# Kernel tuning notes

Hardware: AMD Instinct MI355X
Metric: run time of the kernel (lower is better)

The kernel has to match this reference:

```python
import jax, jax.numpy as jnp
import numpy as np

C = 256
C8 = C // 8


def setup_inputs() -> dict:
    key = jax.random.key(0)
    ks = jax.random.split(key, 9)
    B, H, W = 4, 64, 64
    s = 1.0 / np.sqrt(C)
    return {
        "pre_feat": jax.random.normal(ks[0], (B, C, H, W), jnp.float32),
        "post_feat": jax.random.normal(ks[1], (B, C, H, W), jnp.float32),
        "Wq": jax.random.normal(ks[2], (C8, C), jnp.float32) * s,
        "bq": jnp.zeros((C8,), jnp.float32),
        "Wk": jax.random.normal(ks[3], (C8, C), jnp.float32) * s,
        "bk": jnp.zeros((C8,), jnp.float32),
        "Wv": jax.random.normal(ks[4], (C, C), jnp.float32) * s,
        "bv": jnp.zeros((C,), jnp.float32),
        "gamma": jnp.zeros((1,), jnp.float32),
    }


def reference(pre_feat, post_feat, Wq, bq, Wk, bk, Wv, bv, gamma):
    B, Cc, H, W = pre_feat.shape
    N = H * W
    pre = pre_feat.reshape(B, Cc, N)    # (B, C, N)
    post = post_feat.reshape(B, Cc, N)
    # 1x1 convs == per-pixel linear projections
    q = jnp.einsum('dc,bcn->bdn', Wq, post) + bq[None, :, None]  # (B, C8, N)
    k = jnp.einsum('dc,bcn->bdn', Wk, pre) + bk[None, :, None]   # (B, C8, N)
    v = jnp.einsum('dc,bcn->bdn', Wv, pre) + bv[None, :, None]   # (B, C, N)
    # energy[b,i,j] = <q[b,:,i], k[b,:,j]>  (unscaled)
    energy = jnp.einsum('bdi,bdj->bij', q, k)                    # (B, N, N)
    attention = jax.nn.softmax(energy, axis=-1)
    # out[b,c,i] = sum_j v[b,c,j] * attention[b,i,j]
    out = jnp.einsum('bcj,bij->bci', v, attention).reshape(B, Cc, H, W)
    return gamma[0] * out + post_feat
```

## Files before the change

kernel.cpp:

```cpp
#include <hip/hip_runtime.h>
#include <hip/hip_bf16.h>

#define Bn 4
#define Cn 256
#define Dn 32
#define Nn 4096

typedef __bf16 bf16x8 __attribute__((ext_vector_type(8)));
typedef float f32x4 __attribute__((ext_vector_type(4)));

__device__ __forceinline__ float bf2f(unsigned short u) {
  unsigned int v = ((unsigned int)u) << 16;
  return __builtin_bit_cast(float, v);
}
__device__ __forceinline__ unsigned short f2bf(float f) {
  unsigned int v = __builtin_bit_cast(unsigned int, f);
  v += 0x7FFFu + ((v >> 16) & 1u);
  return (unsigned short)(v >> 16);
}
__device__ __forceinline__ unsigned int pk2(float a, float b) {
  union { __hip_bfloat162 h; unsigned int u; } x;
  x.h = __float22bfloat162_rn(make_float2(a, b));
  return x.u;
}
__device__ __forceinline__ bf16x8 ldfrag(const unsigned short* p) {
  return __builtin_bit_cast(bf16x8, *(const uint4*)p);
}
__device__ __forceinline__ bf16x8 ldfrag_f32(const float* p) {
  float4 a = *(const float4*)p;
  float4 b = *(const float4*)(p + 4);
  union { unsigned int u2[4]; bf16x8 v; } x;
  x.u2[0] = pk2(a.x, a.y); x.u2[1] = pk2(a.z, a.w);
  x.u2[2] = pk2(b.x, b.y); x.u2[3] = pk2(b.z, b.w);
  return x.v;
}
__device__ __forceinline__ void async16(unsigned short* lds, const unsigned short* g) {
  __builtin_amdgcn_global_load_lds(
      (const __attribute__((address_space(1))) unsigned int*)g,
      (__attribute__((address_space(3))) unsigned int*)lds, 16, 0, 0);
}

__global__ __launch_bounds__(256) void qkprep(
    const float* __restrict__ pre, const float* __restrict__ post,
    const float* __restrict__ Wq, const float* __restrict__ bq,
    const float* __restrict__ Wk, const float* __restrict__ bk,
    const float* __restrict__ Wv, const float* __restrict__ bv,
    unsigned short* __restrict__ Qt, unsigned short* __restrict__ Kt,
    unsigned short* __restrict__ VBf)
{
  const int blk = blockIdx.x, tid = threadIdx.x;
  const int lane = tid & 63, w = tid >> 6;
  const int quad = lane >> 4, n16 = lane & 15;
  const f32x4 zz = {0.f, 0.f, 0.f, 0.f};

  if (blk >= 512) {
    __shared__ __align__(16) unsigned short sV[256 * 40];
    const int vb = blk - 512;
    const int b = vb >> 7;
    const int j0 = (vb & 127) << 5;
    const int jsub = w & 1, chalf = w >> 1;
    const int j = j0 + jsub * 16 + n16;

    f32x4 acc[8];
#pragma unroll
    for (int ct = 0; ct < 8; ct++) acc[ct] = zz;

    const float* preB = pre + (size_t)b * Cn * Nn + j;
#pragma unroll
    for (int kc = 0; kc < 8; kc++) {
      const float* pr = preB + (size_t)(kc * 32 + quad * 8) * Nn;
      union { unsigned int u2[4]; bf16x8 v; } bp;
#pragma unroll
      for (int e2 = 0; e2 < 4; e2++) {
        float r0 = pr[(size_t)(2 * e2) * Nn], r1 = pr[(size_t)(2 * e2 + 1) * Nn];
        bp.u2[e2] = pk2(r0, r1);
      }
#pragma unroll
      for (int ct = 0; ct < 8; ct++) {
        bf16x8 aw = ldfrag_f32(Wv + (size_t)(chalf * 128 + ct * 16 + n16) * Cn + kc * 32 + quad * 8);
        acc[ct] = __builtin_amdgcn_mfma_f32_16x16x32_bf16(aw, bp.v, acc[ct], 0, 0, 0);
      }
    }
#pragma unroll
    for (int ct = 0; ct < 8; ct++) {
#pragma unroll
      for (int r = 0; r < 4; r++) {
        const int c = chalf * 128 + ct * 16 + quad * 4 + r;
        sV[c * 40 + jsub * 16 + n16] = f2bf(acc[ct][r] + bv[c]);
      }
    }
    __syncthreads();
#pragma unroll
    for (int k = 0; k < 4; k++) {
      const int slot = tid + k * 256;
      const int c = slot >> 2, seg = slot & 3;
      *(uint4*)(VBf + ((size_t)b * Cn + c) * Nn + j0 + seg * 8) =
          *(const uint4*)(sV + c * 40 + seg * 8);
    }
    return;
  }

  const int b = blk >> 7;
  const int i0 = (blk & 127) << 5;
  const int isub = w & 1, dh = w >> 1;
  const int i = i0 + isub * 16 + n16;

  f32x4 aq = zz, ak = zz;
  const float* postB = post + (size_t)b * Cn * Nn + i;
  const float* preB  = pre  + (size_t)b * Cn * Nn + i;

#pragma unroll
  for (int kc = 0; kc < 8; kc++) {
    const int c0 = kc * 32 + quad * 8;
    const float* pp = postB + (size_t)c0 * Nn;
    const float* pr = preB + (size_t)c0 * Nn;
    union { unsigned int u2[4]; bf16x8 v; } bp, bq8;
#pragma unroll
    for (int e2 = 0; e2 < 4; e2++) {
      float p0 = pp[(size_t)(2 * e2) * Nn], p1 = pp[(size_t)(2 * e2 + 1) * Nn];
      float r0 = pr[(size_t)(2 * e2) * Nn], r1 = pr[(size_t)(2 * e2 + 1) * Nn];
      bp.u2[e2] = pk2(p0, p1);
      bq8.u2[e2] = pk2(r0, r1);
    }
    bf16x8 awq = ldfrag_f32(Wq + (size_t)(dh * 16 + n16) * Cn + kc * 32 + quad * 8);
    bf16x8 awk = ldfrag_f32(Wk + (size_t)(dh * 16 + n16) * Cn + kc * 32 + quad * 8);
    aq = __builtin_amdgcn_mfma_f32_16x16x32_bf16(awq, bp.v, aq, 0, 0, 0);
    ak = __builtin_amdgcn_mfma_f32_16x16x32_bf16(awk, bq8.v, ak, 0, 0, 0);
  }
  const float LOG2E = 1.44269504f;
  union { unsigned short s[4]; uint2 u; } oq, ok;
#pragma unroll
  for (int r = 0; r < 4; r++) {
    int d = dh * 16 + quad * 4 + r;
    oq.s[r] = f2bf((aq[r] + bq[d]) * LOG2E);
    ok.s[r] = f2bf(ak[r] + bk[d]);
  }
  *(uint2*)(Qt + ((size_t)b * Nn + i) * Dn + dh * 16 + quad * 4) = oq.u;
  *(uint2*)(Kt + ((size_t)b * Nn + i) * Dn + dh * 16 + quad * 4) = ok.u;
}

__global__ __launch_bounds__(256, 4) void flash_attn(
    const unsigned short* __restrict__ Qt, const unsigned short* __restrict__ Kt,
    const unsigned short* __restrict__ VBf,
    unsigned short* __restrict__ Opart, float* __restrict__ Lpart)
{
  __shared__ __align__(16) unsigned short sX[256 * 64];
  __shared__ __align__(16) unsigned short Pl[64 * 64];

  const int tid = threadIdx.x;
  const int lane = tid & 63, w = tid >> 6;
  const int quad = lane >> 4, n16 = lane & 15;
  const int b = blockIdx.x >> 8;
  const int js = (blockIdx.x >> 6) & 3;
  const int it = blockIdx.x & 63;
  const int i0 = it * 64;
  const int jbase = js * 1024;

  const bf16x8 qf = ldfrag(Qt + ((size_t)b * Nn + i0 + w * 16 + n16) * Dn + quad * 8);

  const f32x4 zz = {0.f, 0.f, 0.f, 0.f};
  f32x4 acc[4][4];
#pragma unroll
  for (int sub = 0; sub < 4; sub++)
#pragma unroll
    for (int ct = 0; ct < 4; ct++) acc[sub][ct] = zz;
  float lrow = 0.f;

  const size_t laneoff = (size_t)(lane >> 3) * Nn + (size_t)(((lane & 7) ^ (lane >> 3)) << 3);
  const unsigned short* preB = VBf + (size_t)b * Cn * Nn + laneoff;
  const int xsw = n16 & 7;
  const int xoff0 = (quad ^ xsw) << 3;
  const int xoff1 = ((4 + quad) ^ xsw) << 3;
  const int psw = (n16 & 7) << 3;

  for (int t = 0; t < 16; ++t) {
    const int j0 = jbase + t * 64;
    __syncthreads();
#pragma unroll
    for (int k = 0; k < 8; k++) {
      const int rb = (k * 4 + w) * 8;
      async16(sX + rb * 64 + (lane << 3), preB + (size_t)rb * Nn + j0);
    }
    {
      f32x4 sc[4];
#pragma unroll
      for (int jt = 0; jt < 4; jt++) {
        bf16x8 akf = ldfrag(Kt + ((size_t)b * Nn + j0 + jt * 16 + n16) * Dn + quad * 8);
        sc[jt] = __builtin_amdgcn_mfma_f32_16x16x32_bf16(akf, qf, zz, 0, 0, 0);
      }
      float ps = 0.f;
#pragma unroll
      for (int jt = 0; jt < 4; jt++) {
        float p0 = exp2f(fminf(sc[jt][0], 101.f));
        float p1 = exp2f(fminf(sc[jt][1], 101.f));
        float p2 = exp2f(fminf(sc[jt][2], 101.f));
        float p3 = exp2f(fminf(sc[jt][3], 101.f));
        ps += (p0 + p1) + (p2 + p3);
        union { unsigned int u2[2]; uint2 u; } pk;
        pk.u2[0] = pk2(p0, p1);
        pk.u2[1] = pk2(p2, p3);
        *(uint2*)&Pl[(size_t)(w * 16 + n16) * 64 + ((jt * 16 + quad * 4) ^ psw)] = pk.u;
      }
      ps += __shfl_xor(ps, 16);
      ps += __shfl_xor(ps, 32);
      lrow += ps;
    }
    __syncthreads();

#pragma unroll
    for (int kc = 0; kc < 2; kc++) {
      const int xo = kc ? xoff1 : xoff0;
      bf16x8 pB[4];
#pragma unroll
      for (int sub = 0; sub < 4; sub++)
        pB[sub] = ldfrag(&Pl[(size_t)(sub * 16 + n16) * 64 + ((kc * 32 + quad * 8) ^ psw)]);
#pragma unroll
      for (int ct = 0; ct < 4; ct++) {
        const int crow = w * 64 + ct * 16 + n16;
        bf16x8 av = ldfrag(&sX[crow * 64 + xo]);
        acc[0][ct] = __builtin_amdgcn_mfma_f32_16x16x32_bf16(av, pB[0], acc[0][ct], 0, 0, 0);
        acc[1][ct] = __builtin_amdgcn_mfma_f32_16x16x32_bf16(av, pB[1], acc[1][ct], 0, 0, 0);
        acc[2][ct] = __builtin_amdgcn_mfma_f32_16x16x32_bf16(av, pB[2], acc[2][ct], 0, 0, 0);
        acc[3][ct] = __builtin_amdgcn_mfma_f32_16x16x32_bf16(av, pB[3], acc[3][ct], 0, 0, 0);
      }
    }
  }

  const size_t pbase = (size_t)(js * 4 + b) * Nn;
  if (quad == 0) Lpart[pbase + i0 + w * 16 + n16] = lrow;
#pragma unroll
  for (int sub = 0; sub < 4; sub++) {
    const int i = i0 + sub * 16 + n16;
#pragma unroll
    for (int ct = 0; ct < 4; ct++) {
      union { unsigned int u2[2]; uint2 u; } pk;
      pk.u2[0] = pk2(acc[sub][ct][0], acc[sub][ct][1]);
      pk.u2[1] = pk2(acc[sub][ct][2], acc[sub][ct][3]);
      *(uint2*)(Opart + (pbase + i) * 256 + w * 64 + ct * 16 + quad * 4) = pk.u;
    }
  }
}

__global__ __launch_bounds__(256) void combine(
    const unsigned short* __restrict__ Opart, const float* __restrict__ Lpart,
    const float* __restrict__ post, const float* __restrict__ gamma,
    float* __restrict__ out)
{
  __shared__ float sT[64 * 65];
  __shared__ float sL[64];

  const int tid = threadIdx.x;
  const int b = blockIdx.x >> 8;
  const int rest = blockIdx.x & 255;
  const int i0 = (rest >> 2) * 64;
  const int c0 = (rest & 3) * 64;

  if (tid < 64) {
    float l = 0.f;
#pragma unroll
    for (int js = 0; js < 4; js++) l += Lpart[(size_t)(js * 4 + b) * Nn + i0 + tid];
    sL[tid] = 1.f / l;
  }
  __syncthreads();

#pragma unroll
  for (int pass = 0; pass < 2; pass++) {
    const int il = (tid >> 3) + pass * 32;
    const int c8 = (tid & 7) << 3;
    float a[8] = {0.f, 0.f, 0.f, 0.f, 0.f, 0.f, 0.f, 0.f};
#pragma unroll
    for (int js = 0; js < 4; js++) {
      uint4 uu = *(const uint4*)(Opart + ((size_t)(js * 4 + b) * Nn + i0 + il) * 256 + c0 + c8);
      const unsigned short* us = (const unsigned short*)&uu;
#pragma unroll
      for (int e = 0; e < 8; e++) a[e] += bf2f(us[e]);
    }
    const float inv = sL[il];
#pragma unroll
    for (int e = 0; e < 8; e++) sT[(c8 + e) * 65 + il] = a[e] * inv;
  }
  __syncthreads();

  const float g = gamma[0];
#pragma unroll
  for (int itr = 0; itr < 4; itr++) {
    const int slot = tid + itr * 256;
    const int cr = slot >> 4, i4 = (slot & 15) << 2;
    const size_t addr = ((size_t)b * Cn + c0 + cr) * Nn + i0 + i4;
    float4 pp = *(const float4*)(post + addr);
    float4 ov;
    ov.x = g * sT[cr * 65 + i4 + 0] + pp.x;
    ov.y = g * sT[cr * 65 + i4 + 1] + pp.y;
    ov.z = g * sT[cr * 65 + i4 + 2] + pp.z;
    ov.w = g * sT[cr * 65 + i4 + 3] + pp.w;
    *(float4*)(out + addr) = ov;
  }
}

extern "C" void kernel_launch(void* const* d_in, const int* in_sizes, int n_in,
                              void* d_out, int out_size, void* d_ws, size_t ws_size,
                              hipStream_t stream) {
  const float* pre   = (const float*)d_in[0];
  const float* post  = (const float*)d_in[1];
  const float* Wq    = (const float*)d_in[2];
  const float* bq    = (const float*)d_in[3];
  const float* Wk    = (const float*)d_in[4];
  const float* bk    = (const float*)d_in[5];
  const float* Wv    = (const float*)d_in[6];
  const float* bv    = (const float*)d_in[7];
  const float* gamma = (const float*)d_in[8];
  float* out = (float*)d_out;

  unsigned short* ws = (unsigned short*)d_ws;
  unsigned short* Qt    = ws;
  unsigned short* Kt    = Qt + (size_t)Bn * Nn * Dn;
  unsigned short* VBf   = Kt + (size_t)Bn * Nn * Dn;
  float* Lpart = (float*)(VBf + (size_t)Bn * Cn * Nn);
  unsigned short* Opart = (unsigned short*)(Lpart + 4 * Bn * Nn);

  qkprep<<<1024, 256, 0, stream>>>(pre, post, Wq, bq, Wk, bk, Wv, bv,
                                   Qt, Kt, VBf);
  flash_attn<<<1024, 256, 0, stream>>>(Qt, Kt, VBf, Opart, Lpart);
  combine<<<1024, 256, 0, stream>>>(Opart, Lpart, post, gamma, out);
}
```

Baseline: 208.9 us.

## Pre-convert weights to bf16 and fuse V projection into QK prep blocks

Adds a small kernel that converts Wq, Wk and Wv to bf16 once per call, so the projection kernel loads packed bf16 fragments instead of converting fp32 weights inside every block. The V projection is merged into the Q/K blocks, so each block reads the pre features once and computes K and V from the same fragment. The grid drops from 1024 to 512 blocks. In exchange there is an extra kernel launch, higher register pressure from the eight V accumulators living alongside Q/K, and fewer blocks to spread across the GPU.

```diff
diff --git a/kernel.cpp b/kernel.cpp
--- a/kernel.cpp
+++ b/kernel.cpp
@@ -26,13 +26,13 @@
 __device__ __forceinline__ bf16x8 ldfrag(const unsigned short* p) {
   return __builtin_bit_cast(bf16x8, *(const uint4*)p);
 }
-__device__ __forceinline__ bf16x8 ldfrag_f32(const float* p) {
+__device__ __forceinline__ uint4 pack8(const float* p) {
   float4 a = *(const float4*)p;
   float4 b = *(const float4*)(p + 4);
-  union { unsigned int u2[4]; bf16x8 v; } x;
+  union { unsigned int u2[4]; uint4 u; } x;
   x.u2[0] = pk2(a.x, a.y); x.u2[1] = pk2(a.z, a.w);
   x.u2[2] = pk2(b.x, b.y); x.u2[3] = pk2(b.z, b.w);
-  return x.v;
+  return x.u;
 }
 __device__ __forceinline__ void async16(unsigned short* lds, const unsigned short* g) {
   __builtin_amdgcn_global_load_lds(
@@ -40,72 +40,46 @@
       (__attribute__((address_space(3))) unsigned int*)lds, 16, 0, 0);
 }
 
+__global__ __launch_bounds__(256) void wconv(
+    const float* __restrict__ Wq, const float* __restrict__ Wk,
+    const float* __restrict__ Wv,
+    unsigned short* __restrict__ WqBf, unsigned short* __restrict__ WkBf,
+    unsigned short* __restrict__ WvBf)
+{
+  const size_t base = ((size_t)blockIdx.x * 256 + threadIdx.x) * 8;
+  if (base < 8192) {
+    *(uint4*)(WqBf + base) = pack8(Wq + base);
+  } else if (base < 16384) {
+    *(uint4*)(WkBf + base - 8192) = pack8(Wk + base - 8192);
+  } else {
+    *(uint4*)(WvBf + base - 16384) = pack8(Wv + base - 16384);
+  }
+}
+
 __global__ __launch_bounds__(256) void qkprep(
     const float* __restrict__ pre, const float* __restrict__ post,
-    const float* __restrict__ Wq, const float* __restrict__ bq,
-    const float* __restrict__ Wk, const float* __restrict__ bk,
-    const float* __restrict__ Wv, const float* __restrict__ bv,
+    const unsigned short* __restrict__ WqBf, const float* __restrict__ bq,
+    const unsigned short* __restrict__ WkBf, const float* __restrict__ bk,
+    const unsigned short* __restrict__ WvBf, const float* __restrict__ bv,
     unsigned short* __restrict__ Qt, unsigned short* __restrict__ Kt,
     unsigned short* __restrict__ VBf)
 {
-  const int blk = blockIdx.x, tid = threadIdx.x;
+  __shared__ __align__(16) unsigned short sV[256 * 40];
+
+  const int tid = threadIdx.x;
   const int lane = tid & 63, w = tid >> 6;
   const int quad = lane >> 4, n16 = lane & 15;
-  const f32x4 zz = {0.f, 0.f, 0.f, 0.f};
-
-  if (blk >= 512) {
-    __shared__ __align__(16) unsigned short sV[256 * 40];
-    const int vb = blk - 512;
-    const int b = vb >> 7;
-    const int j0 = (vb & 127) << 5;
-    const int jsub = w & 1, chalf = w >> 1;
-    const int j = j0 + jsub * 16 + n16;
-
-    f32x4 acc[8];
-#pragma unroll
-    for (int ct = 0; ct < 8; ct++) acc[ct] = zz;
-
-    const float* preB = pre + (size_t)b * Cn * Nn + j;
-#pragma unroll
-    for (int kc = 0; kc < 8; kc++) {
-      const float* pr = preB + (size_t)(kc * 32 + quad * 8) * Nn;
-      union { unsigned int u2[4]; bf16x8 v; } bp;
-#pragma unroll
-      for (int e2 = 0; e2 < 4; e2++) {
-        float r0 = pr[(size_t)(2 * e2) * Nn], r1 = pr[(size_t)(2 * e2 + 1) * Nn];
-        bp.u2[e2] = pk2(r0, r1);
-      }
-#pragma unroll
-      for (int ct = 0; ct < 8; ct++) {
-        bf16x8 aw = ldfrag_f32(Wv + (size_t)(chalf * 128 + ct * 16 + n16) * Cn + kc * 32 + quad * 8);
-        acc[ct] = __builtin_amdgcn_mfma_f32_16x16x32_bf16(aw, bp.v, acc[ct], 0, 0, 0);
-      }
-    }
-#pragma unroll
-    for (int ct = 0; ct < 8; ct++) {
-#pragma unroll
-      for (int r = 0; r < 4; r++) {
-        const int c = chalf * 128 + ct * 16 + quad * 4 + r;
-        sV[c * 40 + jsub * 16 + n16] = f2bf(acc[ct][r] + bv[c]);
-      }
-    }
-    __syncthreads();
-#pragma unroll
-    for (int k = 0; k < 4; k++) {
-      const int slot = tid + k * 256;
-      const int c = slot >> 2, seg = slot & 3;
-      *(uint4*)(VBf + ((size_t)b * Cn + c) * Nn + j0 + seg * 8) =
-          *(const uint4*)(sV + c * 40 + seg * 8);
-    }
-    return;
-  }
-
-  const int b = blk >> 7;
-  const int i0 = (blk & 127) << 5;
+  const int b = blockIdx.x >> 7;
+  const int i0 = (blockIdx.x & 127) << 5;
   const int isub = w & 1, dh = w >> 1;
   const int i = i0 + isub * 16 + n16;
 
+  const f32x4 zz = {0.f, 0.f, 0.f, 0.f};
   f32x4 aq = zz, ak = zz;
+  f32x4 accv[8];
+#pragma unroll
+  for (int ct = 0; ct < 8; ct++) accv[ct] = zz;
+
   const float* postB = post + (size_t)b * Cn * Nn + i;
   const float* preB  = pre  + (size_t)b * Cn * Nn + i;
 
@@ -122,11 +96,17 @@
       bp.u2[e2] = pk2(p0, p1);
       bq8.u2[e2] = pk2(r0, r1);
     }
-    bf16x8 awq = ldfrag_f32(Wq + (size_t)(dh * 16 + n16) * Cn + kc * 32 + quad * 8);
-    bf16x8 awk = ldfrag_f32(Wk + (size_t)(dh * 16 + n16) * Cn + kc * 32 + quad * 8);
+    bf16x8 awq = ldfrag(WqBf + (size_t)(dh * 16 + n16) * Cn + kc * 32 + quad * 8);
+    bf16x8 awk = ldfrag(WkBf + (size_t)(dh * 16 + n16) * Cn + kc * 32 + quad * 8);
     aq = __builtin_amdgcn_mfma_f32_16x16x32_bf16(awq, bp.v, aq, 0, 0, 0);
     ak = __builtin_amdgcn_mfma_f32_16x16x32_bf16(awk, bq8.v, ak, 0, 0, 0);
-  }
+#pragma unroll
+    for (int ct = 0; ct < 8; ct++) {
+      bf16x8 aw = ldfrag(WvBf + (size_t)(dh * 128 + ct * 16 + n16) * Cn + kc * 32 + quad * 8);
+      accv[ct] = __builtin_amdgcn_mfma_f32_16x16x32_bf16(aw, bq8.v, accv[ct], 0, 0, 0);
+    }
+  }
+
   const float LOG2E = 1.44269504f;
   union { unsigned short s[4]; uint2 u; } oq, ok;
 #pragma unroll
@@ -137,6 +117,23 @@
   }
   *(uint2*)(Qt + ((size_t)b * Nn + i) * Dn + dh * 16 + quad * 4) = oq.u;
   *(uint2*)(Kt + ((size_t)b * Nn + i) * Dn + dh * 16 + quad * 4) = ok.u;
+
+#pragma unroll
+  for (int ct = 0; ct < 8; ct++) {
+#pragma unroll
+    for (int r = 0; r < 4; r++) {
+      const int c = dh * 128 + ct * 16 + quad * 4 + r;
+      sV[c * 40 + isub * 16 + n16] = f2bf(accv[ct][r] + bv[c]);
+    }
+  }
+  __syncthreads();
+#pragma unroll
+  for (int k = 0; k < 4; k++) {
+    const int slot = tid + k * 256;
+    const int c = slot >> 2, seg = slot & 3;
+    *(uint4*)(VBf + ((size_t)b * Cn + c) * Nn + i0 + seg * 8) =
+        *(const uint4*)(sV + c * 40 + seg * 8);
+  }
 }
 
 __global__ __launch_bounds__(256, 4) void flash_attn(
@@ -315,11 +312,15 @@
   unsigned short* Qt    = ws;
   unsigned short* Kt    = Qt + (size_t)Bn * Nn * Dn;
   unsigned short* VBf   = Kt + (size_t)Bn * Nn * Dn;
-  float* Lpart = (float*)(VBf + (size_t)Bn * Cn * Nn);
+  unsigned short* WqBf  = VBf + (size_t)Bn * Cn * Nn;
+  unsigned short* WkBf  = WqBf + Dn * Cn;
+  unsigned short* WvBf  = WkBf + Dn * Cn;
+  float* Lpart = (float*)(WvBf + Cn * Cn);
   unsigned short* Opart = (unsigned short*)(Lpart + 4 * Bn * Nn);
 
-  qkprep<<<1024, 256, 0, stream>>>(pre, post, Wq, bq, Wk, bk, Wv, bv,
-                                   Qt, Kt, VBf);
+  wconv<<<40, 256, 0, stream>>>(Wq, Wk, Wv, WqBf, WkBf, WvBf);
+  qkprep<<<512, 256, 0, stream>>>(pre, post, WqBf, bq, WkBf, bk, WvBf, bv,
+                                  Qt, Kt, VBf);
   flash_attn<<<1024, 256, 0, stream>>>(Qt, Kt, VBf, Opart, Lpart);
   combine<<<1024, 256, 0, stream>>>(Opart, Lpart, post, gamma, out);
 }
```

Result: faster. 186.9 us (-10.5%).
